# Kernel tuning notes

Hardware: AMD Instinct MI355X
Metric: run time of the kernel (lower is better)

Reference implementation:

```python
import jax, jax.numpy as jnp
import numpy as np

M1, N1, M2, N2 = 32, 64, 24, 48  # Kronecker block dims; 32*24=768, 64*48=3072


def setup_inputs() -> dict:
    key = jax.random.key(0)
    k1, k2, k3, k4, k5 = jax.random.split(key, 5)
    rank = 64
    x = jax.random.normal(k1, (4, 4096, 768), dtype=jnp.float32)
    A_factors = jax.random.normal(k2, (M1 * N1, rank), dtype=jnp.float32) * 0.05
    B_factors = jax.random.normal(k3, (rank, M2 * N2), dtype=jnp.float32) * 0.05
    # 'Sparse' residual is materialized dense in the original module (to_dense()).
    Sparse = jax.random.normal(k4, (768, 3072), dtype=jnp.float32) * 0.02
    bias = jax.random.normal(k5, (3072,), dtype=jnp.float32) * 0.02
    return {"x": x, "A_factors": A_factors, "B_factors": B_factors,
            "Sparse": Sparse, "bias": bias}


def reference(x, A_factors, B_factors, Sparse, bias):
    # Low-rank product: [2048, r] @ [r, 1152] -> [2048, 1152]
    W_tilde = A_factors @ B_factors
    # Kronecker permute: (m1, n1, m2, n2) -> (m1, m2, n1, n2) -> [768, 3072]
    W_low = W_tilde.reshape(M1, N1, M2, N2).transpose(0, 2, 1, 3).reshape(
        M1 * M2, N1 * N2)
    W = W_low + Sparse
    # Dense GEMM: [B, S, 768] @ [768, 3072] + bias
    return x @ W + bias
```

## Files before the change

kernel.cpp:

```cpp
#include <hip/hip_runtime.h>
#include <hip/hip_bf16.h>
#include <stdint.h>

#define M_TOT 16384
#define N_TOT 3072
#define K_TOT 768

#define BM 256
#define BN 256
#define BK 32
#define NT (K_TOT / BK)

typedef __attribute__((ext_vector_type(8))) short short8;
typedef __attribute__((ext_vector_type(4))) float f32x4;

__device__ __forceinline__ unsigned short f2bf(float f) {
    union { float f; unsigned u; } v;
    v.f = f;
    unsigned r = v.u + 0x7FFFu + ((v.u >> 16) & 1u);
    return (unsigned short)(r >> 16);
}

__global__ __launch_bounds__(256) void cvt_x_kernel(const float* __restrict__ x,
                                                    unsigned short* __restrict__ xb,
                                                    int n8) {
    int i = blockIdx.x * blockDim.x + threadIdx.x;
    int stride = gridDim.x * blockDim.x;
    const float4* xv = reinterpret_cast<const float4*>(x);
    uint4* ov = reinterpret_cast<uint4*>(xb);
    for (; i < n8; i += stride) {
        float4 a = xv[2 * i], b = xv[2 * i + 1];
        uint4 o;
        o.x = (unsigned)f2bf(a.x) | ((unsigned)f2bf(a.y) << 16);
        o.y = (unsigned)f2bf(a.z) | ((unsigned)f2bf(a.w) << 16);
        o.z = (unsigned)f2bf(b.x) | ((unsigned)f2bf(b.y) << 16);
        o.w = (unsigned)f2bf(b.z) | ((unsigned)f2bf(b.w) << 16);
        ov[i] = o;
    }
}

__global__ __launch_bounds__(256) void wtilde_gemm_kernel(const float* __restrict__ Af,
                                                          const float* __restrict__ Bf,
                                                          float* __restrict__ Wtmp) {
    __shared__ float As[64][68];
    __shared__ float Bs[64][68];
    const int tid = threadIdx.x;
    const int bp = blockIdx.x / 18, bq = blockIdx.x % 18;
    const int p0 = bp * 64, q0 = bq * 64;
    {
        #pragma unroll
        for (int i = 0; i < 4; ++i) {
            int idx = i * 256 + tid;
            int row = idx >> 4, c4 = (idx & 15) * 4;
            f32x4 v = *reinterpret_cast<const f32x4*>(&Af[(size_t)(p0 + row) * 64 + c4]);
            As[c4 + 0][row] = v[0]; As[c4 + 1][row] = v[1];
            As[c4 + 2][row] = v[2]; As[c4 + 3][row] = v[3];
        }
    }
    {
        #pragma unroll
        for (int l = 0; l < 4; ++l) {
            int idx = l * 256 + tid;
            int k = idx >> 4, c4 = (idx & 15) * 4;
            *reinterpret_cast<f32x4*>(&Bs[k][c4]) =
                *reinterpret_cast<const f32x4*>(&Bf[(size_t)k * 1152 + q0 + c4]);
        }
    }
    __syncthreads();
    float acc[4][4] = {};
    const int rb = (tid >> 4) * 4;
    const int cb = (tid & 15) * 4;
    #pragma unroll
    for (int k = 0; k < 64; ++k) {
        f32x4 a = *reinterpret_cast<const f32x4*>(&As[k][rb]);
        f32x4 b = *reinterpret_cast<const f32x4*>(&Bs[k][cb]);
        #pragma unroll
        for (int i = 0; i < 4; ++i)
            #pragma unroll
            for (int j = 0; j < 4; ++j)
                acc[i][j] = fmaf(a[i], b[j], acc[i][j]);
    }
    #pragma unroll
    for (int i = 0; i < 4; ++i) {
        f32x4 o = {acc[i][0], acc[i][1], acc[i][2], acc[i][3]};
        *reinterpret_cast<f32x4*>(&Wtmp[(size_t)(p0 + rb + i) * 1152 + q0 + cb]) = o;
    }
}

__global__ __launch_bounds__(256) void permute_w_kernel(const float* __restrict__ Wtmp,
                                                        const float* __restrict__ Sp,
                                                        unsigned short* __restrict__ Wt) {
    __shared__ float T[64][65];
    const int tid = threadIdx.x;
    const int r0 = (blockIdx.x % 12) * 64;
    const int c0 = (blockIdx.x / 12) * 64;
    #pragma unroll
    for (int l = 0; l < 16; ++l) {
        int i = l * 4 + (tid >> 6);
        int j = tid & 63;
        int r = r0 + i, c = c0 + j;
        int m1 = r / 24, m2 = r - m1 * 24;
        int n1 = c / 48, n2 = c - n1 * 48;
        T[i][j] = Wtmp[(size_t)(m1 * 64 + n1) * 1152 + m2 * 48 + n2]
                + Sp[(size_t)r * 3072 + c];
    }
    __syncthreads();
    #pragma unroll
    for (int u0 = 0; u0 < 2; ++u0) {
        int u = u0 * 256 + tid;
        int jj = u >> 3;
        int ii = u & 7;
        unsigned w[4];
        #pragma unroll
        for (int t = 0; t < 4; ++t) {
            unsigned lo = f2bf(T[ii * 8 + 2 * t][jj]);
            unsigned hi = f2bf(T[ii * 8 + 2 * t + 1][jj]);
            w[t] = lo | (hi << 16);
        }
        uint4 o = {w[0], w[1], w[2], w[3]};
        *reinterpret_cast<uint4*>(&Wt[(size_t)(c0 + jj) * 768 + r0 + ii * 8]) = o;
    }
}

__device__ __forceinline__ void gld16(const void* g, void* l) {
    __builtin_amdgcn_global_load_lds(
        (const __attribute__((address_space(1))) void*)g,
        (__attribute__((address_space(3))) void*)l, 16, 0, 0);
}

__global__ __launch_bounds__(512, 2) void gemm_bt_kernel(
    const unsigned short* __restrict__ A, const unsigned short* __restrict__ Bt,
    const float* __restrict__ bias, float* __restrict__ C) {
    __shared__ unsigned short As[4][BM * BK];
    __shared__ unsigned short Bs[4][BN * BK];

    const int tid = threadIdx.x;
    const int lane = tid & 63;
    const int wid = tid >> 6;
    const int wr = wid >> 2;
    const int wc = wid & 3;

    const int wg = (blockIdx.x & 7) * 96 + (blockIdx.x >> 3);
    const int bm = wg / (N_TOT / BN), bn = wg % (N_TOT / BN);
    const int brow = bm * BM, bcol = bn * BN;

    const int srow = tid >> 2;
    const int soff = (((tid & 3) ^ ((tid >> 3) & 3)) << 4);
    const char* pA = (const char*)A + ((size_t)(brow + srow) * K_TOT) * 2 + soff;
    const char* pB = (const char*)Bt + ((size_t)(bcol + srow) * K_TOT) * 2 + soff;
    const size_t row128 = (size_t)128 * K_TOT * 2;
    const int tid16 = tid * 16;

#define STAGE_AH(u) do { const char* s_ = pA + (size_t)(u) * (BK * 2);           \
        gld16(s_,          (char*)&As[(u) & 3][0] + tid16);                      \
        gld16(s_ + row128, (char*)&As[(u) & 3][0] + tid16 + 8192); } while (0)
#define STAGE_BH(u) do { const char* s_ = pB + (size_t)(u) * (BK * 2);           \
        gld16(s_,          (char*)&Bs[(u) & 3][0] + tid16);                      \
        gld16(s_ + row128, (char*)&Bs[(u) & 3][0] + tid16 + 8192); } while (0)

    const int la = lane & 15;
    const int g4 = lane >> 4;
    const int swb = ((g4 ^ ((lane >> 1) & 3)) << 4);
#define FRAG_A(bu, r) (*(const short8*)((const char*)&As[bu][0] + (r) * 64 + swb))
#define FRAG_B(bu, r) (*(const short8*)((const char*)&Bs[bu][0] + (r) * 64 + swb))

#define LGKM0_FENCE() do {                                                       \
        asm volatile("s_waitcnt lgkmcnt(0)" ::: "memory");                       \
        __builtin_amdgcn_sched_barrier(0); } while (0)

    f32x4 acc[8][4];
    #pragma unroll
    for (int m = 0; m < 8; ++m)
        #pragma unroll
        for (int n = 0; n < 4; ++n)
            acc[m][n] = (f32x4){0.f, 0.f, 0.f, 0.f};

    STAGE_AH(0); STAGE_BH(0);
    STAGE_AH(1); STAGE_BH(1);
    STAGE_AH(2); STAGE_BH(2);
    asm volatile("s_waitcnt vmcnt(8)" ::: "memory");
    __builtin_amdgcn_s_barrier();

    const int arow = wr * 128;
    const int bcolw = wc * 64;
    for (int t = 0; t < NT; ++t) {
        const int bu = t & 3;
        short8 a0[4], b0[4];
        #pragma unroll
        for (int n = 0; n < 4; ++n) b0[n] = FRAG_B(bu, bcolw + n * 16 + la);
        #pragma unroll
        for (int m = 0; m < 4; ++m) a0[m] = FRAG_A(bu, arow + m * 16 + la);
        if (t < NT - 3) STAGE_AH(t + 3);
        __builtin_amdgcn_s_barrier();
        LGKM0_FENCE();
        __builtin_amdgcn_s_setprio(1);
        #pragma unroll
        for (int m = 0; m < 4; ++m)
            #pragma unroll
            for (int n = 0; n < 4; ++n)
                acc[m][n] = __builtin_amdgcn_mfma_f32_16x16x32_bf16(
                    b0[n], a0[m], acc[m][n], 0, 0, 0);
        __builtin_amdgcn_s_setprio(0);
        __builtin_amdgcn_s_barrier();
        #pragma unroll
        for (int m = 0; m < 4; ++m) a0[m] = FRAG_A(bu, arow + 64 + m * 16 + la);
        if (t < NT - 3) STAGE_BH(t + 3);
        if (t < NT - 3)       asm volatile("s_waitcnt vmcnt(8)" ::: "memory");
        else if (t == NT - 3) asm volatile("s_waitcnt vmcnt(4)" ::: "memory");
        else if (t == NT - 2) asm volatile("s_waitcnt vmcnt(0)" ::: "memory");
        __builtin_amdgcn_s_barrier();
        LGKM0_FENCE();
        __builtin_amdgcn_s_setprio(1);
        #pragma unroll
        for (int m = 0; m < 4; ++m)
            #pragma unroll
            for (int n = 0; n < 4; ++n)
                acc[4 + m][n] = __builtin_amdgcn_mfma_f32_16x16x32_bf16(
                    b0[n], a0[m], acc[4 + m][n], 0, 0, 0);
        __builtin_amdgcn_s_setprio(0);
        __builtin_amdgcn_s_barrier();
    }

    #pragma unroll
    for (int n = 0; n < 4; ++n) {
        const int gc = bcol + bcolw + n * 16 + g4 * 4;
        const f32x4 bv = *reinterpret_cast<const f32x4*>(&bias[gc]);
        #pragma unroll
        for (int m = 0; m < 8; ++m) {
            const int gr = brow + arow + m * 16 + la;
            f32x4 o = {acc[m][n][0] + bv[0], acc[m][n][1] + bv[1],
                       acc[m][n][2] + bv[2], acc[m][n][3] + bv[3]};
            *reinterpret_cast<f32x4*>(&C[(size_t)gr * N_TOT + gc]) = o;
        }
    }
#undef STAGE_AH
#undef STAGE_BH
#undef FRAG_A
#undef FRAG_B
#undef LGKM0_FENCE
}

extern "C" void kernel_launch(void* const* d_in, const int* in_sizes, int n_in,
                              void* d_out, int out_size, void* d_ws, size_t ws_size,
                              hipStream_t stream) {
    const float* x    = (const float*)d_in[0];
    const float* Af   = (const float*)d_in[1];
    const float* Bf   = (const float*)d_in[2];
    const float* Sp   = (const float*)d_in[3];
    const float* bias = (const float*)d_in[4];
    float* out = (float*)d_out;

    unsigned short* xb = (unsigned short*)d_ws;
    unsigned short* wt = xb + (size_t)M_TOT * K_TOT;
    float* wtmp = (float*)d_out;

    hipLaunchKernelGGL(cvt_x_kernel, dim3(2048), dim3(256), 0, stream,
                       x, xb, M_TOT * K_TOT / 8);
    hipLaunchKernelGGL(wtilde_gemm_kernel, dim3(32 * 18), dim3(256), 0, stream,
                       Af, Bf, wtmp);
    hipLaunchKernelGGL(permute_w_kernel, dim3(12 * 48), dim3(256), 0, stream,
                       wtmp, Sp, wt);
    hipLaunchKernelGGL(gemm_bt_kernel,
                       dim3((M_TOT / BM) * (N_TOT / BN)), dim3(512),
                       0, stream, xb, wt, bias, out);
}
```

Measured before the change: 151.0 us.

## Fuse low-rank W build, permute and x conversion into one prep kernel

Replaces the three preprocessing kernels (x fp32->bf16 conversion, low-rank A@B GEMM, Kronecker permute+sparse add) with a single kernel whose blocks are split by index between the two jobs. The W blocks compute four rows of A@B directly into shared memory and immediately permute, add the sparse residual and write bf16 transposed W, removing the fp32 intermediate round trip through global memory. This cuts two kernel launches and the Wtmp traffic, at the cost of a less efficient rank-64 GEMM that rereads Bf from global memory in each block and uncoalesced strided Sp reads.

```diff
diff --git a/kernel.cpp b/kernel.cpp
--- a/kernel.cpp
+++ b/kernel.cpp
@@ -21,104 +21,76 @@
     return (unsigned short)(r >> 16);
 }
 
-__global__ __launch_bounds__(256) void cvt_x_kernel(const float* __restrict__ x,
-                                                    unsigned short* __restrict__ xb,
-                                                    int n8) {
-    int i = blockIdx.x * blockDim.x + threadIdx.x;
-    int stride = gridDim.x * blockDim.x;
-    const float4* xv = reinterpret_cast<const float4*>(x);
-    uint4* ov = reinterpret_cast<uint4*>(xb);
-    for (; i < n8; i += stride) {
-        float4 a = xv[2 * i], b = xv[2 * i + 1];
-        uint4 o;
-        o.x = (unsigned)f2bf(a.x) | ((unsigned)f2bf(a.y) << 16);
-        o.y = (unsigned)f2bf(a.z) | ((unsigned)f2bf(a.w) << 16);
-        o.z = (unsigned)f2bf(b.x) | ((unsigned)f2bf(b.y) << 16);
-        o.w = (unsigned)f2bf(b.z) | ((unsigned)f2bf(b.w) << 16);
-        ov[i] = o;
-    }
-}
-
-__global__ __launch_bounds__(256) void wtilde_gemm_kernel(const float* __restrict__ Af,
-                                                          const float* __restrict__ Bf,
-                                                          float* __restrict__ Wtmp) {
-    __shared__ float As[64][68];
-    __shared__ float Bs[64][68];
+__global__ __launch_bounds__(384) void prep_cvt_kernel(
+    const float* __restrict__ Af, const float* __restrict__ Bf,
+    const float* __restrict__ Sp, const float* __restrict__ x,
+    unsigned short* __restrict__ xb, unsigned short* __restrict__ Wt) {
+    __shared__ float a_sh[4][64];
+    __shared__ float wrow[4][1160];
     const int tid = threadIdx.x;
-    const int bp = blockIdx.x / 18, bq = blockIdx.x % 18;
-    const int p0 = bp * 64, q0 = bq * 64;
-    {
-        #pragma unroll
-        for (int i = 0; i < 4; ++i) {
-            int idx = i * 256 + tid;
-            int row = idx >> 4, c4 = (idx & 15) * 4;
-            f32x4 v = *reinterpret_cast<const f32x4*>(&Af[(size_t)(p0 + row) * 64 + c4]);
-            As[c4 + 0][row] = v[0]; As[c4 + 1][row] = v[1];
-            As[c4 + 2][row] = v[2]; As[c4 + 3][row] = v[3];
-        }
-    }
-    {
-        #pragma unroll
-        for (int l = 0; l < 4; ++l) {
-            int idx = l * 256 + tid;
-            int k = idx >> 4, c4 = (idx & 15) * 4;
-            *reinterpret_cast<f32x4*>(&Bs[k][c4]) =
-                *reinterpret_cast<const f32x4*>(&Bf[(size_t)k * 1152 + q0 + c4]);
-        }
-    }
-    __syncthreads();
-    float acc[4][4] = {};
-    const int rb = (tid >> 4) * 4;
-    const int cb = (tid & 15) * 4;
-    #pragma unroll
-    for (int k = 0; k < 64; ++k) {
-        f32x4 a = *reinterpret_cast<const f32x4*>(&As[k][rb]);
-        f32x4 b = *reinterpret_cast<const f32x4*>(&Bs[k][cb]);
-        #pragma unroll
-        for (int i = 0; i < 4; ++i)
-            #pragma unroll
-            for (int j = 0; j < 4; ++j)
-                acc[i][j] = fmaf(a[i], b[j], acc[i][j]);
-    }
-    #pragma unroll
-    for (int i = 0; i < 4; ++i) {
-        f32x4 o = {acc[i][0], acc[i][1], acc[i][2], acc[i][3]};
-        *reinterpret_cast<f32x4*>(&Wtmp[(size_t)(p0 + rb + i) * 1152 + q0 + cb]) = o;
-    }
-}
-
-__global__ __launch_bounds__(256) void permute_w_kernel(const float* __restrict__ Wtmp,
-                                                        const float* __restrict__ Sp,
-                                                        unsigned short* __restrict__ Wt) {
-    __shared__ float T[64][65];
-    const int tid = threadIdx.x;
-    const int r0 = (blockIdx.x % 12) * 64;
-    const int c0 = (blockIdx.x / 12) * 64;
-    #pragma unroll
-    for (int l = 0; l < 16; ++l) {
-        int i = l * 4 + (tid >> 6);
-        int j = tid & 63;
-        int r = r0 + i, c = c0 + j;
-        int m1 = r / 24, m2 = r - m1 * 24;
-        int n1 = c / 48, n2 = c - n1 * 48;
-        T[i][j] = Wtmp[(size_t)(m1 * 64 + n1) * 1152 + m2 * 48 + n2]
-                + Sp[(size_t)r * 3072 + c];
-    }
-    __syncthreads();
-    #pragma unroll
-    for (int u0 = 0; u0 < 2; ++u0) {
-        int u = u0 * 256 + tid;
-        int jj = u >> 3;
-        int ii = u & 7;
-        unsigned w[4];
-        #pragma unroll
-        for (int t = 0; t < 4; ++t) {
-            unsigned lo = f2bf(T[ii * 8 + 2 * t][jj]);
-            unsigned hi = f2bf(T[ii * 8 + 2 * t + 1][jj]);
-            w[t] = lo | (hi << 16);
-        }
-        uint4 o = {w[0], w[1], w[2], w[3]};
-        *reinterpret_cast<uint4*>(&Wt[(size_t)(c0 + jj) * 768 + r0 + ii * 8]) = o;
+    const int b = blockIdx.x;
+
+    if (b < 512) {
+        const int m1 = b >> 4;
+        const int n10 = (b & 15) * 4;
+        if (tid < 256) {
+            int rr = tid >> 6, k = tid & 63;
+            a_sh[rr][k] = Af[(size_t)(m1 * 64 + n10 + rr) * 64 + k];
+        }
+        __syncthreads();
+        float acc[4][3] = {};
+        #pragma unroll 2
+        for (int k = 0; k < 64; ++k) {
+            const float* brow = Bf + (size_t)k * 1152;
+            float b0 = brow[tid], b1 = brow[tid + 384], b2 = brow[tid + 768];
+            #pragma unroll
+            for (int rr = 0; rr < 4; ++rr) {
+                float a = a_sh[rr][k];
+                acc[rr][0] = fmaf(a, b0, acc[rr][0]);
+                acc[rr][1] = fmaf(a, b1, acc[rr][1]);
+                acc[rr][2] = fmaf(a, b2, acc[rr][2]);
+            }
+        }
+        #pragma unroll
+        for (int rr = 0; rr < 4; ++rr) {
+            wrow[rr][tid] = acc[rr][0];
+            wrow[rr][tid + 384] = acc[rr][1];
+            wrow[rr][tid + 768] = acc[rr][2];
+        }
+        __syncthreads();
+        if (tid < 192) {
+            const int rr = tid / 48, n2 = tid % 48;
+            const int c = (n10 + rr) * 48 + n2;
+            const int r0 = m1 * 24;
+            unsigned w[12];
+            #pragma unroll
+            for (int t2 = 0; t2 < 12; ++t2) {
+                float lo = wrow[rr][(2 * t2) * 48 + n2]
+                         + Sp[(size_t)(r0 + 2 * t2) * 3072 + c];
+                float hi = wrow[rr][(2 * t2 + 1) * 48 + n2]
+                         + Sp[(size_t)(r0 + 2 * t2 + 1) * 3072 + c];
+                w[t2] = (unsigned)f2bf(lo) | ((unsigned)f2bf(hi) << 16);
+            }
+            uint4* d4 = reinterpret_cast<uint4*>(Wt + (size_t)c * 768 + r0);
+            d4[0] = (uint4){w[0], w[1], w[2], w[3]};
+            d4[1] = (uint4){w[4], w[5], w[6], w[7]};
+            d4[2] = (uint4){w[8], w[9], w[10], w[11]};
+        }
+    } else {
+        const int n8 = M_TOT * K_TOT / 8;
+        int i = (b - 512) * 384 + tid;
+        const int stride = 2048 * 384;
+        const float4* xv = reinterpret_cast<const float4*>(x);
+        uint4* ov = reinterpret_cast<uint4*>(xb);
+        for (; i < n8; i += stride) {
+            float4 a = xv[2 * i], c = xv[2 * i + 1];
+            uint4 o;
+            o.x = (unsigned)f2bf(a.x) | ((unsigned)f2bf(a.y) << 16);
+            o.y = (unsigned)f2bf(a.z) | ((unsigned)f2bf(a.w) << 16);
+            o.z = (unsigned)f2bf(c.x) | ((unsigned)f2bf(c.y) << 16);
+            o.w = (unsigned)f2bf(c.z) | ((unsigned)f2bf(c.w) << 16);
+            ov[i] = o;
+        }
     }
 }
 
@@ -252,14 +224,9 @@
 
     unsigned short* xb = (unsigned short*)d_ws;
     unsigned short* wt = xb + (size_t)M_TOT * K_TOT;
-    float* wtmp = (float*)d_out;
-
-    hipLaunchKernelGGL(cvt_x_kernel, dim3(2048), dim3(256), 0, stream,
-                       x, xb, M_TOT * K_TOT / 8);
-    hipLaunchKernelGGL(wtilde_gemm_kernel, dim3(32 * 18), dim3(256), 0, stream,
-                       Af, Bf, wtmp);
-    hipLaunchKernelGGL(permute_w_kernel, dim3(12 * 48), dim3(256), 0, stream,
-                       wtmp, Sp, wt);
+
+    hipLaunchKernelGGL(prep_cvt_kernel, dim3(512 + 2048), dim3(384), 0, stream,
+                       Af, Bf, Sp, x, xb, wt);
     hipLaunchKernelGGL(gemm_bt_kernel,
                        dim3((M_TOT / BM) * (N_TOT / BN)), dim3(512),
                        0, stream, xb, wt, bias, out);
```

Result: faster. 127.5 us (-15.6%).
